# Kernel optimization log

Measured on AMD Instinct MI355X. Metric: run time of the kernel, lower is better.

## Reference

```python
import jax, jax.numpy as jnp
import numpy as np

B, S, D, H = 2, 2048, 1024, 16
HD = D // H            # head_dim = 64
CHUNK = 1024           # hard-coded in the torch module
ROPE_THETA = 10000.0


def setup_inputs() -> dict:
    key = jax.random.key(0)
    ks = jax.random.split(key, 5)
    hidden_states = jax.random.normal(ks[0], (B, S, D), dtype=jnp.float32)
    # Precomputed RoPE frequencies: freqs_cis[s, j] = exp(i * s * theta_j),
    # stored as real [S, HD//2, 2] = (cos, sin).
    inv_freq = 1.0 / (ROPE_THETA ** (np.arange(0, HD, 2, dtype=np.float32) / HD))
    ang = np.outer(np.arange(S, dtype=np.float32), inv_freq)  # [S, HD//2]
    freqs_cis = jnp.stack([jnp.cos(ang), jnp.sin(ang)], axis=-1).astype(jnp.float32)
    scale = 0.02
    Wq = jax.random.normal(ks[1], (D, D), dtype=jnp.float32) * scale
    Wk = jax.random.normal(ks[2], (D, D), dtype=jnp.float32) * scale
    Wv = jax.random.normal(ks[3], (D, D), dtype=jnp.float32) * scale
    Wo = jax.random.normal(ks[4], (D, D), dtype=jnp.float32) * scale
    return {"hidden_states": hidden_states, "freqs_cis": freqs_cis,
            "Wq": Wq, "Wk": Wk, "Wv": Wv, "Wo": Wo}


def _apply_rope(x, freqs_cis):
    # x: [B, S, H, HD]; freqs_cis: [S, HD//2, 2] (cos, sin)
    b, s, h, hd = x.shape
    xr = x.reshape(b, s, h, hd // 2, 2)
    a, bb = xr[..., 0], xr[..., 1]
    c = freqs_cis[:s, :, 0][None, :, None, :]  # broadcast over batch, heads
    d = freqs_cis[:s, :, 1][None, :, None, :]
    # complex multiply (a + ib)(c + id)
    out = jnp.stack([a * c - bb * d, a * d + bb * c], axis=-1)
    return out.reshape(b, s, h, hd)


def reference(hidden_states, freqs_cis, Wq, Wk, Wv, Wo):
    b, s, dm = hidden_states.shape
    q = (hidden_states @ Wq).reshape(b, s, H, HD)
    k = (hidden_states @ Wk).reshape(b, s, H, HD)
    v = (hidden_states @ Wv).reshape(b, s, H, HD)
    q = _apply_rope(q, freqs_cis)
    k = _apply_rope(k, freqs_cis)
    q = q.transpose(0, 2, 1, 3)  # [B, H, S, HD]
    k = k.transpose(0, 2, 1, 3)
    v = v.transpose(0, 2, 1, 3)
    scaling = HD ** (-0.5)
    out = jnp.zeros_like(q)
    # Faithful replication of the (buggy) chunked attention: softmax is
    # normalized PER key-chunk, then chunk outputs are summed.
    for i in range(0, s, CHUNK):
        j = min(i + CHUNK, s)
        w = jnp.einsum('bhqd,bhkd->bhqk', q, k[:, :, i:j]) * scaling
        w = jax.nn.softmax(w.astype(jnp.float32), axis=-1).astype(q.dtype)
        out = out + jnp.einsum('bhqk,bhkd->bhqd', w, v[:, :, i:j])
    out = out.transpose(0, 2, 1, 3).reshape(b, s, dm)
    return out @ Wo
```

## Files before the change

kernel.cpp:

```cpp
#include <hip/hip_runtime.h>
#include <hip/hip_bf16.h>
#include <cstdint>

typedef __bf16 bf16x8 __attribute__((ext_vector_type(8)));
typedef float f32x4 __attribute__((ext_vector_type(4)));
typedef float f32x16 __attribute__((ext_vector_type(16)));

#define MFMA16(a, b, c) __builtin_amdgcn_mfma_f32_16x16x32_bf16(a, b, c, 0, 0, 0)
#define MFMA32(a, b, c) __builtin_amdgcn_mfma_f32_32x32x16_bf16(a, b, c, 0, 0, 0)

__device__ __forceinline__ void gload_lds16(const void* g, void* l) {
  __builtin_amdgcn_global_load_lds(
      (const __attribute__((address_space(1))) unsigned int*)g,
      (__attribute__((address_space(3))) unsigned int*)l, 16, 0, 0);
}

__device__ __forceinline__ unsigned short f2bf(float x) {
  union { float f; uint32_t u; } v; v.f = x;
  uint32_t r = v.u + 0x7fff + ((v.u >> 16) & 1);
  return (unsigned short)(r >> 16);
}
__device__ __forceinline__ float bf2f(unsigned short h) {
  union { float f; uint32_t u; } v; v.u = ((uint32_t)h) << 16;
  return v.f;
}
__device__ __forceinline__ f32x16 fzero16() {
  f32x16 v;
#pragma unroll
  for (int i = 0; i < 16; ++i) v[i] = 0.f;
  return v;
}

__global__ __launch_bounds__(256) void k_split(const float* __restrict__ x,
                                               unsigned short* __restrict__ hi, int n4) {
  int i = blockIdx.x * blockDim.x + threadIdx.x;
  if (i >= n4) return;
  float4 v = ((const float4*)x)[i];
  ushort4 h;
  h.x = f2bf(v.x); h.y = f2bf(v.y); h.z = f2bf(v.z); h.w = f2bf(v.w);
  ((ushort4*)hi)[i] = h;
}

__global__ __launch_bounds__(256) void k_wsplit(
    const float* __restrict__ Wq, const float* __restrict__ Wk,
    const float* __restrict__ Wv, const float* __restrict__ Wo,
    unsigned short* __restrict__ WtqH, unsigned short* __restrict__ WtkH,
    unsigned short* __restrict__ WtvH, unsigned short* __restrict__ WtoH) {
  const int z = blockIdx.z;
  const float* W = (z == 0) ? Wq : (z == 1) ? Wk : (z == 2) ? Wv : Wo;
  unsigned short* WtH = (z == 0) ? WtqH : (z == 1) ? WtkH : (z == 2) ? WtvH : WtoH;
  __shared__ float tile[32][33];
  const int bx = blockIdx.x, by = blockIdx.y;
  const int tx = threadIdx.x & 31, ty = threadIdx.x >> 5;
#pragma unroll
  for (int i = 0; i < 4; ++i)
    tile[ty + i * 8][tx] = W[(size_t)(by * 32 + ty + i * 8) * 1024 + bx * 32 + tx];
  __syncthreads();
#pragma unroll
  for (int i = 0; i < 4; ++i) {
    float v = tile[tx][ty + i * 8];
    WtH[(size_t)(bx * 32 + ty + i * 8) * 1024 + by * 32 + tx] = f2bf(v);
  }
}

__global__ __launch_bounds__(256, 2) void k_qkv(
    const unsigned short* __restrict__ hsH,
    const unsigned short* __restrict__ WqH, const unsigned short* __restrict__ WkH,
    const unsigned short* __restrict__ WvH, const float* __restrict__ freqs,
    unsigned short* __restrict__ qB, unsigned short* __restrict__ kB,
    unsigned short* __restrict__ vB) {
  __shared__ unsigned short Ah[128 * 32], Bh[128 * 32];
  const int tid = threadIdx.x;
  const int bm = blockIdx.y, bn = blockIdx.x;
  const int w = bn >> 3;
  const int n0 = (bn & 7) * 128;
  const unsigned short* WH = (w == 0) ? WqH : (w == 1) ? WkH : WvH;
  const int lane = tid & 63, wave = tid >> 6;
  const int wm = (wave & 1) * 64, wn = (wave >> 1) * 64;
  const int l15 = lane & 15, lq = lane >> 4;

  f32x4 acc[4][4];
#pragma unroll
  for (int i = 0; i < 4; i++)
#pragma unroll
    for (int j = 0; j < 4; j++) acc[i][j] = (f32x4){0.f, 0.f, 0.f, 0.f};

  const char* baseA = (const char*)hsH + (size_t)(bm * 128) * 2048;
  const char* baseB = (const char*)WH + (size_t)n0 * 2048;
  const int off0 = tid << 4, row0 = off0 >> 6, seg0 = off0 & 63;
  const int off1 = (tid + 256) << 4, row1 = off1 >> 6, seg1 = off1 & 63;

  for (int k0 = 0; k0 < 1024; k0 += 32) {
    __syncthreads();
    gload_lds16(baseA + (size_t)row0 * 2048 + k0 * 2 + seg0, (char*)Ah + wave * 1024);
    gload_lds16(baseB + (size_t)row0 * 2048 + k0 * 2 + seg0, (char*)Bh + wave * 1024);
    gload_lds16(baseA + (size_t)row1 * 2048 + k0 * 2 + seg1,
                (char*)Ah + 4096 + wave * 1024);
    gload_lds16(baseB + (size_t)row1 * 2048 + k0 * 2 + seg1,
                (char*)Bh + 4096 + wave * 1024);
    __syncthreads();
    bf16x8 ah[4], bh[4];
#pragma unroll
    for (int i = 0; i < 4; ++i) {
      ah[i] = *(const bf16x8*)&Ah[(wm + i * 16 + l15) * 32 + lq * 8];
      bh[i] = *(const bf16x8*)&Bh[(wn + i * 16 + l15) * 32 + lq * 8];
    }
#pragma unroll
    for (int i = 0; i < 4; ++i)
#pragma unroll
      for (int j = 0; j < 4; ++j) acc[i][j] = MFMA16(ah[i], bh[j], acc[i][j]);
  }

  unsigned short* dst = (w == 0) ? qB : (w == 1) ? kB : vB;
#pragma unroll
  for (int i = 0; i < 4; ++i) {
#pragma unroll
    for (int j = 0; j < 4; ++j) {
      int colw = n0 + wn + j * 16 + l15;
      int h = colw >> 6, d = colw & 63;
#pragma unroll
      for (int r = 0; r < 4; ++r) {
        int rowg = bm * 128 + wm + i * 16 + lq * 4 + r;
        int s = rowg & 2047, b = rowg >> 11;
        float val = acc[i][j][r];
        if (w < 2) {
          float partner = __shfl_xor(val, 1);
          int jj = d >> 1;
          float cs = freqs[(s * 32 + jj) * 2 + 0];
          float sn = freqs[(s * 32 + jj) * 2 + 1];
          float res = (d & 1) ? (partner * sn + val * cs) : (val * cs - partner * sn);
          dst[(((size_t)(b * 16 + h)) * 2048 + s) * 64 + d] = f2bf(res);
        } else {
          dst[(((size_t)(b * 16 + h)) * 64 + d) * 2048 + s] = f2bf(val);
        }
      }
    }
  }
}

#define LDP 72

__global__ __launch_bounds__(256, 2) void k_attn(
    const unsigned short* __restrict__ qB, const unsigned short* __restrict__ kB,
    const unsigned short* __restrict__ vB,
    unsigned short* __restrict__ c0, unsigned short* __restrict__ c1) {
  __shared__ unsigned short Pt[4 * 64 * LDP];
  const int tid = threadIdx.x, lane = tid & 63, wave = tid >> 6;
  const int l31 = lane & 31, lh = lane >> 5;
  const int bid = blockIdx.x;
  const int x = (bid >> 3) & 7;
  const int gg = (bid & 7) + 8 * (bid >> 6);
  const int bh = gg & 31;
  const int chunk = gg >> 5;
  const int q0 = x * 256 + wave * 64;
  const size_t base = (size_t)bh * 2048 * 64;
  const float sc = 0.125f * 1.44269504089f;

  bf16x8 qf[2][4];
#pragma unroll
  for (int qt = 0; qt < 2; ++qt)
#pragma unroll
    for (int ks = 0; ks < 4; ++ks)
      qf[qt][ks] = *(const bf16x8*)(qB + base + (size_t)(q0 + qt * 32 + l31) * 64 +
                                    ks * 16 + lh * 8);

  const unsigned short* kp = kB + base + (size_t)chunk * 1024 * 64 + l31 * 64 + lh * 8;
  const unsigned short* vp = vB + base + l31 * 2048 + chunk * 1024 + lh * 8;
  unsigned short* Pw = Pt + wave * (64 * LDP);

  bf16x8 kfa[4], kfb[4];
#pragma unroll
  for (int ks = 0; ks < 4; ++ks) {
    kfa[ks] = *(const bf16x8*)(kp + ks * 16);
    kfb[ks] = *(const bf16x8*)(kp + 2048 + ks * 16);
  }
  kp += 4096;

  f32x16 o[2][2];
#pragma unroll
  for (int a = 0; a < 2; ++a)
#pragma unroll
    for (int bq = 0; bq < 2; ++bq) o[a][bq] = fzero16();
  float rsum[2] = {0.f, 0.f};

  for (int kb = 0; kb < 16; ++kb) {
    bf16x8 vf[2][4];
#pragma unroll
    for (int dt = 0; dt < 2; ++dt)
#pragma unroll
      for (int ks = 0; ks < 4; ++ks)
        vf[dt][ks] = *(const bf16x8*)(vp + dt * 65536 + ks * 16);

#pragma unroll
    for (int mt = 0; mt < 2; ++mt) {
      f32x16 s0 = fzero16(), s1 = fzero16();
      if (mt == 0) {
#pragma unroll
        for (int ks = 0; ks < 4; ++ks) {
          s0 = MFMA32(kfa[ks], qf[0][ks], s0);
          s1 = MFMA32(kfa[ks], qf[1][ks], s1);
        }
#pragma unroll
        for (int ks = 0; ks < 4; ++ks) kfa[ks] = *(const bf16x8*)(kp + ks * 16);
      } else {
#pragma unroll
        for (int ks = 0; ks < 4; ++ks) {
          s0 = MFMA32(kfb[ks], qf[0][ks], s0);
          s1 = MFMA32(kfb[ks], qf[1][ks], s1);
        }
#pragma unroll
        for (int ks = 0; ks < 4; ++ks)
          kfb[ks] = *(const bf16x8*)(kp + 2048 + ks * 16);
      }
#pragma unroll
      for (int qt = 0; qt < 2; ++qt) {
        const f32x16& sv = qt ? s1 : s0;
        float ps[16];
        float rs = 0.f;
#pragma unroll
        for (int r = 0; r < 16; ++r) {
          ps[r] = __builtin_exp2f(sv[r] * sc);
          rs += ps[r];
        }
        rsum[qt] += rs;
        unsigned int* prow =
            (unsigned int*)(Pw + (qt * 32 + l31) * LDP + mt * 32 + 4 * lh);
#pragma unroll
        for (int p = 0; p < 8; ++p) {
          union { unsigned int u; __bf16 h2[2]; } pk;
          pk.h2[0] = (__bf16)ps[2 * p];
          pk.h2[1] = (__bf16)ps[2 * p + 1];
          prow[4 * (p >> 1) + (p & 1)] = pk.u;
        }
      }
    }
    kp += 4096;

#pragma unroll
    for (int qt = 0; qt < 2; ++qt)
#pragma unroll
      for (int ks = 0; ks < 4; ++ks) {
        bf16x8 pf = *(const bf16x8*)(Pw + (qt * 32 + l31) * LDP + ks * 16 + lh * 8);
        o[0][qt] = MFMA32(vf[0][ks], pf, o[0][qt]);
        o[1][qt] = MFMA32(vf[1][ks], pf, o[1][qt]);
      }
    vp += 64;
  }

  unsigned short* cB = chunk ? c1 : c0;
  const int b = bh >> 4, h = bh & 15;
#pragma unroll
  for (int qt = 0; qt < 2; ++qt) {
    float lsum = rsum[qt] + __shfl_xor(rsum[qt], 32);
    float inv = 1.f / lsum;
    int s = q0 + qt * 32 + l31;
#pragma unroll
    for (int dt = 0; dt < 2; ++dt)
#pragma unroll
      for (int g = 0; g < 4; ++g) {
        int d = dt * 32 + 4 * lh + 8 * g;
        size_t idx = ((size_t)(b * 2048 + s)) * 1024 + h * 64 + d;
        ushort4 hv;
#pragma unroll
        for (int t = 0; t < 4; ++t)
          ((unsigned short*)&hv)[t] = f2bf(o[dt][qt][g * 4 + t] * inv);
        *(ushort4*)(cB + idx) = hv;
      }
  }
}

__global__ __launch_bounds__(256) void k_comb(const unsigned short* __restrict__ c0,
                                              const unsigned short* __restrict__ c1,
                                              unsigned short* __restrict__ outB,
                                              int n8) {
  int i = blockIdx.x * blockDim.x + threadIdx.x;
  if (i >= n8) return;
  uint4 a = ((const uint4*)c0)[i];
  uint4 b = ((const uint4*)c1)[i];
  uint4 r;
  const unsigned short* pa = (const unsigned short*)&a;
  const unsigned short* pb = (const unsigned short*)&b;
  unsigned short* pr = (unsigned short*)&r;
#pragma unroll
  for (int j = 0; j < 8; ++j) pr[j] = f2bf(bf2f(pa[j]) + bf2f(pb[j]));
  ((uint4*)outB)[i] = r;
}

__global__ __launch_bounds__(256, 2) void k_out(const unsigned short* __restrict__ A,
                                                const unsigned short* __restrict__ B,
                                                float* __restrict__ out) {
  __shared__ unsigned short Ah[128 * 32], Bh[128 * 32];
  const int tid = threadIdx.x;
  const int bm = blockIdx.y, n0 = blockIdx.x * 128;
  const int lane = tid & 63, wave = tid >> 6;
  const int wm = (wave & 1) * 64, wn = (wave >> 1) * 64;
  const int l15 = lane & 15, lq = lane >> 4;

  f32x4 acc[4][4];
#pragma unroll
  for (int i = 0; i < 4; i++)
#pragma unroll
    for (int j = 0; j < 4; j++) acc[i][j] = (f32x4){0.f, 0.f, 0.f, 0.f};

  const char* baseA = (const char*)A + (size_t)(bm * 128) * 2048;
  const char* baseB = (const char*)B + (size_t)n0 * 2048;
  const int off0 = tid << 4, row0 = off0 >> 6, seg0 = off0 & 63;
  const int off1 = (tid + 256) << 4, row1 = off1 >> 6, seg1 = off1 & 63;

  for (int k0 = 0; k0 < 1024; k0 += 32) {
    __syncthreads();
    gload_lds16(baseA + (size_t)row0 * 2048 + k0 * 2 + seg0, (char*)Ah + wave * 1024);
    gload_lds16(baseB + (size_t)row0 * 2048 + k0 * 2 + seg0, (char*)Bh + wave * 1024);
    gload_lds16(baseA + (size_t)row1 * 2048 + k0 * 2 + seg1,
                (char*)Ah + 4096 + wave * 1024);
    gload_lds16(baseB + (size_t)row1 * 2048 + k0 * 2 + seg1,
                (char*)Bh + 4096 + wave * 1024);
    __syncthreads();
    bf16x8 ah[4], bh[4];
#pragma unroll
    for (int i = 0; i < 4; ++i) {
      ah[i] = *(const bf16x8*)&Ah[(wm + i * 16 + l15) * 32 + lq * 8];
      bh[i] = *(const bf16x8*)&Bh[(wn + i * 16 + l15) * 32 + lq * 8];
    }
#pragma unroll
    for (int i = 0; i < 4; ++i)
#pragma unroll
      for (int j = 0; j < 4; ++j) acc[i][j] = MFMA16(ah[i], bh[j], acc[i][j]);
  }
#pragma unroll
  for (int i = 0; i < 4; ++i)
#pragma unroll
    for (int j = 0; j < 4; ++j) {
      int colw = n0 + wn + j * 16 + l15;
#pragma unroll
      for (int r = 0; r < 4; ++r) {
        int rowg = bm * 128 + wm + i * 16 + lq * 4 + r;
        out[(size_t)rowg * 1024 + colw] = acc[i][j][r];
      }
    }
}

extern "C" void kernel_launch(void* const* d_in, const int* in_sizes, int n_in,
                              void* d_out, int out_size, void* d_ws, size_t ws_size,
                              hipStream_t stream) {
  const float* hs = (const float*)d_in[0];
  const float* freqs = (const float*)d_in[1];
  const float* Wq = (const float*)d_in[2];
  const float* Wk = (const float*)d_in[3];
  const float* Wv = (const float*)d_in[4];
  const float* Wo = (const float*)d_in[5];
  float* out = (float*)d_out;

  const size_t MD = (size_t)4096 * 1024;
  const size_t WW = (size_t)1024 * 1024;
  unsigned short* hsH = (unsigned short*)d_ws;
  unsigned short* WtqH = hsH + MD;
  unsigned short* WtkH = WtqH + WW;
  unsigned short* WtvH = WtkH + WW;
  unsigned short* WtoH = WtvH + WW;
  unsigned short* qB = WtoH + WW;
  unsigned short* kB = qB + MD;
  unsigned short* vB = kB + MD;
  unsigned short* c0 = vB + MD;
  unsigned short* c1 = c0 + MD;
  unsigned short* attnB = hsH;

  k_split<<<4096, 256, 0, stream>>>(hs, hsH, (int)(MD / 4));
  k_wsplit<<<dim3(32, 32, 4), 256, 0, stream>>>(Wq, Wk, Wv, Wo,
                                                WtqH, WtkH, WtvH, WtoH);
  k_qkv<<<dim3(24, 32), 256, 0, stream>>>(hsH, WtqH, WtkH, WtvH, freqs, qB, kB, vB);
  k_attn<<<512, 256, 0, stream>>>(qB, kB, vB, c0, c1);
  k_comb<<<2048, 256, 0, stream>>>(c0, c1, attnB, (int)(MD / 8));
  k_out<<<dim3(8, 32), 256, 0, stream>>>(attnB, WtoH, out);
}
```

Before: 261.0 us.

## Halve per-wave query tile in attention kernel and double grid size

Each attention wave now handles 32 query rows instead of 64, which halves the accumulator and score registers and the LDS P tile. The grid doubles to 1024 blocks and the launch bounds ask for 4 blocks per CU, raising occupancy and parallelism. In exchange every K and V fragment loaded from global memory is reused across only half as many queries, so K/V load traffic per output doubles.

```diff
diff --git a/kernel.cpp b/kernel.cpp
--- a/kernel.cpp
+++ b/kernel.cpp
@@ -140,33 +140,30 @@
 
 #define LDP 72
 
-__global__ __launch_bounds__(256, 2) void k_attn(
+__global__ __launch_bounds__(256, 4) void k_attn(
     const unsigned short* __restrict__ qB, const unsigned short* __restrict__ kB,
     const unsigned short* __restrict__ vB,
     unsigned short* __restrict__ c0, unsigned short* __restrict__ c1) {
-  __shared__ unsigned short Pt[4 * 64 * LDP];
+  __shared__ unsigned short Pt[4 * 32 * LDP];
   const int tid = threadIdx.x, lane = tid & 63, wave = tid >> 6;
   const int l31 = lane & 31, lh = lane >> 5;
   const int bid = blockIdx.x;
-  const int x = (bid >> 3) & 7;
-  const int gg = (bid & 7) + 8 * (bid >> 6);
+  const int x = (bid >> 3) & 15;
+  const int gg = (bid & 7) + 8 * (bid >> 7);
   const int bh = gg & 31;
   const int chunk = gg >> 5;
-  const int q0 = x * 256 + wave * 64;
+  const int q0 = x * 128 + wave * 32;
   const size_t base = (size_t)bh * 2048 * 64;
   const float sc = 0.125f * 1.44269504089f;
 
-  bf16x8 qf[2][4];
-#pragma unroll
-  for (int qt = 0; qt < 2; ++qt)
-#pragma unroll
-    for (int ks = 0; ks < 4; ++ks)
-      qf[qt][ks] = *(const bf16x8*)(qB + base + (size_t)(q0 + qt * 32 + l31) * 64 +
-                                    ks * 16 + lh * 8);
+  bf16x8 qf[4];
+#pragma unroll
+  for (int ks = 0; ks < 4; ++ks)
+    qf[ks] = *(const bf16x8*)(qB + base + (size_t)(q0 + l31) * 64 + ks * 16 + lh * 8);
 
   const unsigned short* kp = kB + base + (size_t)chunk * 1024 * 64 + l31 * 64 + lh * 8;
   const unsigned short* vp = vB + base + l31 * 2048 + chunk * 1024 + lh * 8;
-  unsigned short* Pw = Pt + wave * (64 * LDP);
+  unsigned short* Pw = Pt + wave * (32 * LDP);
 
   bf16x8 kfa[4], kfb[4];
 #pragma unroll
@@ -176,12 +173,10 @@
   }
   kp += 4096;
 
-  f32x16 o[2][2];
-#pragma unroll
-  for (int a = 0; a < 2; ++a)
-#pragma unroll
-    for (int bq = 0; bq < 2; ++bq) o[a][bq] = fzero16();
-  float rsum[2] = {0.f, 0.f};
+  f32x16 o[2];
+#pragma unroll
+  for (int a = 0; a < 2; ++a) o[a] = fzero16();
+  float rsum = 0.f;
 
   for (int kb = 0; kb < 16; ++kb) {
     bf16x8 vf[2][4];
@@ -193,80 +188,64 @@
 
 #pragma unroll
     for (int mt = 0; mt < 2; ++mt) {
-      f32x16 s0 = fzero16(), s1 = fzero16();
+      f32x16 s0 = fzero16();
       if (mt == 0) {
 #pragma unroll
-        for (int ks = 0; ks < 4; ++ks) {
-          s0 = MFMA32(kfa[ks], qf[0][ks], s0);
-          s1 = MFMA32(kfa[ks], qf[1][ks], s1);
-        }
+        for (int ks = 0; ks < 4; ++ks) s0 = MFMA32(kfa[ks], qf[ks], s0);
 #pragma unroll
         for (int ks = 0; ks < 4; ++ks) kfa[ks] = *(const bf16x8*)(kp + ks * 16);
       } else {
 #pragma unroll
-        for (int ks = 0; ks < 4; ++ks) {
-          s0 = MFMA32(kfb[ks], qf[0][ks], s0);
-          s1 = MFMA32(kfb[ks], qf[1][ks], s1);
-        }
+        for (int ks = 0; ks < 4; ++ks) s0 = MFMA32(kfb[ks], qf[ks], s0);
 #pragma unroll
         for (int ks = 0; ks < 4; ++ks)
           kfb[ks] = *(const bf16x8*)(kp + 2048 + ks * 16);
       }
-#pragma unroll
-      for (int qt = 0; qt < 2; ++qt) {
-        const f32x16& sv = qt ? s1 : s0;
-        float ps[16];
-        float rs = 0.f;
-#pragma unroll
-        for (int r = 0; r < 16; ++r) {
-          ps[r] = __builtin_exp2f(sv[r] * sc);
-          rs += ps[r];
-        }
-        rsum[qt] += rs;
-        unsigned int* prow =
-            (unsigned int*)(Pw + (qt * 32 + l31) * LDP + mt * 32 + 4 * lh);
-#pragma unroll
-        for (int p = 0; p < 8; ++p) {
-          union { unsigned int u; __bf16 h2[2]; } pk;
-          pk.h2[0] = (__bf16)ps[2 * p];
-          pk.h2[1] = (__bf16)ps[2 * p + 1];
-          prow[4 * (p >> 1) + (p & 1)] = pk.u;
-        }
+      float ps[16];
+      float rs = 0.f;
+#pragma unroll
+      for (int r = 0; r < 16; ++r) {
+        ps[r] = __builtin_exp2f(s0[r] * sc);
+        rs += ps[r];
+      }
+      rsum += rs;
+      unsigned int* prow = (unsigned int*)(Pw + l31 * LDP + mt * 32 + 4 * lh);
+#pragma unroll
+      for (int p = 0; p < 8; ++p) {
+        union { unsigned int u; __bf16 h2[2]; } pk;
+        pk.h2[0] = (__bf16)ps[2 * p];
+        pk.h2[1] = (__bf16)ps[2 * p + 1];
+        prow[4 * (p >> 1) + (p & 1)] = pk.u;
       }
     }
     kp += 4096;
 
 #pragma unroll
-    for (int qt = 0; qt < 2; ++qt)
-#pragma unroll
-      for (int ks = 0; ks < 4; ++ks) {
-        bf16x8 pf = *(const bf16x8*)(Pw + (qt * 32 + l31) * LDP + ks * 16 + lh * 8);
-        o[0][qt] = MFMA32(vf[0][ks], pf, o[0][qt]);
-        o[1][qt] = MFMA32(vf[1][ks], pf, o[1][qt]);
-      }
+    for (int ks = 0; ks < 4; ++ks) {
+      bf16x8 pf = *(const bf16x8*)(Pw + l31 * LDP + ks * 16 + lh * 8);
+      o[0] = MFMA32(vf[0][ks], pf, o[0]);
+      o[1] = MFMA32(vf[1][ks], pf, o[1]);
+    }
     vp += 64;
   }
 
   unsigned short* cB = chunk ? c1 : c0;
   const int b = bh >> 4, h = bh & 15;
-#pragma unroll
-  for (int qt = 0; qt < 2; ++qt) {
-    float lsum = rsum[qt] + __shfl_xor(rsum[qt], 32);
-    float inv = 1.f / lsum;
-    int s = q0 + qt * 32 + l31;
-#pragma unroll
-    for (int dt = 0; dt < 2; ++dt)
-#pragma unroll
-      for (int g = 0; g < 4; ++g) {
-        int d = dt * 32 + 4 * lh + 8 * g;
-        size_t idx = ((size_t)(b * 2048 + s)) * 1024 + h * 64 + d;
-        ushort4 hv;
-#pragma unroll
-        for (int t = 0; t < 4; ++t)
-          ((unsigned short*)&hv)[t] = f2bf(o[dt][qt][g * 4 + t] * inv);
-        *(ushort4*)(cB + idx) = hv;
-      }
-  }
+  float lsum = rsum + __shfl_xor(rsum, 32);
+  float inv = 1.f / lsum;
+  int s = q0 + l31;
+#pragma unroll
+  for (int dt = 0; dt < 2; ++dt)
+#pragma unroll
+    for (int g = 0; g < 4; ++g) {
+      int d = dt * 32 + 4 * lh + 8 * g;
+      size_t idx = ((size_t)(b * 2048 + s)) * 1024 + h * 64 + d;
+      ushort4 hv;
+#pragma unroll
+      for (int t = 0; t < 4; ++t)
+        ((unsigned short*)&hv)[t] = f2bf(o[dt][g * 4 + t] * inv);
+      *(ushort4*)(cB + idx) = hv;
+    }
 }
 
 __global__ __launch_bounds__(256) void k_comb(const unsigned short* __restrict__ c0,
@@ -369,7 +348,7 @@
   k_wsplit<<<dim3(32, 32, 4), 256, 0, stream>>>(Wq, Wk, Wv, Wo,
                                                 WtqH, WtkH, WtvH, WtoH);
   k_qkv<<<dim3(24, 32), 256, 0, stream>>>(hsH, WtqH, WtkH, WtvH, freqs, qB, kB, vB);
-  k_attn<<<512, 256, 0, stream>>>(qB, kB, vB, c0, c1);
+  k_attn<<<1024, 256, 0, stream>>>(qB, kB, vB, c0, c1);
   k_comb<<<2048, 256, 0, stream>>>(c0, c1, attnB, (int)(MD / 8));
   k_out<<<dim3(8, 32), 256, 0, stream>>>(attnB, WtoH, out);
 }
```

Result: slower. 324.6 us (+24.4%).

## Feed softmax probabilities directly from registers to PV MFMA via permuted V layout

Applied to the files above, without the earlier changes.

The attention kernel no longer round-trips the probability tile through LDS. The V tensor is written with a permuted sequence index (bits 2 and 3 swapped), so the QK^T MFMA accumulator layout matches the B-operand layout needed by the PV MFMA. The softmax scale (1/8·log2e) is folded into Q at projection time, which removes a multiply per score. This cuts LDS writes, LDS reads and the associated waits, at the cost of a fragile layout coupling between the projection and attention kernels.

```diff
diff --git a/kernel.cpp b/kernel.cpp
--- a/kernel.cpp
+++ b/kernel.cpp
@@ -29,6 +29,23 @@
 #pragma unroll
   for (int i = 0; i < 16; ++i) v[i] = 0.f;
   return v;
+}
+
+__device__ __forceinline__ void ptrans(const f32x16& sv, float& rsum,
+                                       bf16x8& f0, bf16x8& f1) {
+  float ps[16];
+#pragma unroll
+  for (int r = 0; r < 16; ++r) ps[r] = __builtin_exp2f(sv[r]);
+  float rs = 0.f;
+#pragma unroll
+  for (int r = 0; r < 16; ++r) rs += ps[r];
+  rsum += rs;
+  bf16x8 a, b;
+#pragma unroll
+  for (int r = 0; r < 8; ++r) a[r] = (__bf16)ps[r];
+#pragma unroll
+  for (int r = 0; r < 8; ++r) b[r] = (__bf16)ps[8 + r];
+  f0 = a; f1 = b;
 }
 
 __global__ __launch_bounds__(256) void k_split(const float* __restrict__ x,
@@ -129,22 +146,21 @@
           float cs = freqs[(s * 32 + jj) * 2 + 0];
           float sn = freqs[(s * 32 + jj) * 2 + 1];
           float res = (d & 1) ? (partner * sn + val * cs) : (val * cs - partner * sn);
+          if (w == 0) res *= 0.18033688011112042f;
           dst[(((size_t)(b * 16 + h)) * 2048 + s) * 64 + d] = f2bf(res);
         } else {
-          dst[(((size_t)(b * 16 + h)) * 64 + d) * 2048 + s] = f2bf(val);
+          int sp = (s & ~12) | ((s & 4) << 1) | ((s & 8) >> 1);
+          dst[(((size_t)(b * 16 + h)) * 64 + d) * 2048 + sp] = f2bf(val);
         }
       }
     }
   }
 }
-
-#define LDP 72
 
 __global__ __launch_bounds__(256, 2) void k_attn(
     const unsigned short* __restrict__ qB, const unsigned short* __restrict__ kB,
     const unsigned short* __restrict__ vB,
     unsigned short* __restrict__ c0, unsigned short* __restrict__ c1) {
-  __shared__ unsigned short Pt[4 * 64 * LDP];
   const int tid = threadIdx.x, lane = tid & 63, wave = tid >> 6;
   const int l31 = lane & 31, lh = lane >> 5;
   const int bid = blockIdx.x;
@@ -154,7 +170,6 @@
   const int chunk = gg >> 5;
   const int q0 = x * 256 + wave * 64;
   const size_t base = (size_t)bh * 2048 * 64;
-  const float sc = 0.125f * 1.44269504089f;
 
   bf16x8 qf[2][4];
 #pragma unroll
@@ -166,7 +181,6 @@
 
   const unsigned short* kp = kB + base + (size_t)chunk * 1024 * 64 + l31 * 64 + lh * 8;
   const unsigned short* vp = vB + base + l31 * 2048 + chunk * 1024 + lh * 8;
-  unsigned short* Pw = Pt + wave * (64 * LDP);
 
   bf16x8 kfa[4], kfb[4];
 #pragma unroll
@@ -191,59 +205,49 @@
       for (int ks = 0; ks < 4; ++ks)
         vf[dt][ks] = *(const bf16x8*)(vp + dt * 65536 + ks * 16);
 
-#pragma unroll
-    for (int mt = 0; mt < 2; ++mt) {
+    bf16x8 f0, f1;
+    {
       f32x16 s0 = fzero16(), s1 = fzero16();
-      if (mt == 0) {
-#pragma unroll
-        for (int ks = 0; ks < 4; ++ks) {
-          s0 = MFMA32(kfa[ks], qf[0][ks], s0);
-          s1 = MFMA32(kfa[ks], qf[1][ks], s1);
-        }
-#pragma unroll
-        for (int ks = 0; ks < 4; ++ks) kfa[ks] = *(const bf16x8*)(kp + ks * 16);
-      } else {
-#pragma unroll
-        for (int ks = 0; ks < 4; ++ks) {
-          s0 = MFMA32(kfb[ks], qf[0][ks], s0);
-          s1 = MFMA32(kfb[ks], qf[1][ks], s1);
-        }
-#pragma unroll
-        for (int ks = 0; ks < 4; ++ks)
-          kfb[ks] = *(const bf16x8*)(kp + 2048 + ks * 16);
-      }
-#pragma unroll
-      for (int qt = 0; qt < 2; ++qt) {
-        const f32x16& sv = qt ? s1 : s0;
-        float ps[16];
-        float rs = 0.f;
-#pragma unroll
-        for (int r = 0; r < 16; ++r) {
-          ps[r] = __builtin_exp2f(sv[r] * sc);
-          rs += ps[r];
-        }
-        rsum[qt] += rs;
-        unsigned int* prow =
-            (unsigned int*)(Pw + (qt * 32 + l31) * LDP + mt * 32 + 4 * lh);
-#pragma unroll
-        for (int p = 0; p < 8; ++p) {
-          union { unsigned int u; __bf16 h2[2]; } pk;
-          pk.h2[0] = (__bf16)ps[2 * p];
-          pk.h2[1] = (__bf16)ps[2 * p + 1];
-          prow[4 * (p >> 1) + (p & 1)] = pk.u;
-        }
-      }
+#pragma unroll
+      for (int ks = 0; ks < 4; ++ks) {
+        s0 = MFMA32(kfa[ks], qf[0][ks], s0);
+        s1 = MFMA32(kfa[ks], qf[1][ks], s1);
+      }
+#pragma unroll
+      for (int ks = 0; ks < 4; ++ks) kfa[ks] = *(const bf16x8*)(kp + ks * 16);
+      ptrans(s0, rsum[0], f0, f1);
+      o[0][0] = MFMA32(vf[0][0], f0, o[0][0]);
+      o[1][0] = MFMA32(vf[1][0], f0, o[1][0]);
+      o[0][0] = MFMA32(vf[0][1], f1, o[0][0]);
+      o[1][0] = MFMA32(vf[1][1], f1, o[1][0]);
+      ptrans(s1, rsum[1], f0, f1);
+      o[0][1] = MFMA32(vf[0][0], f0, o[0][1]);
+      o[1][1] = MFMA32(vf[1][0], f0, o[1][1]);
+      o[0][1] = MFMA32(vf[0][1], f1, o[0][1]);
+      o[1][1] = MFMA32(vf[1][1], f1, o[1][1]);
+    }
+    {
+      f32x16 s0 = fzero16(), s1 = fzero16();
+#pragma unroll
+      for (int ks = 0; ks < 4; ++ks) {
+        s0 = MFMA32(kfb[ks], qf[0][ks], s0);
+        s1 = MFMA32(kfb[ks], qf[1][ks], s1);
+      }
+#pragma unroll
+      for (int ks = 0; ks < 4; ++ks)
+        kfb[ks] = *(const bf16x8*)(kp + 2048 + ks * 16);
+      ptrans(s0, rsum[0], f0, f1);
+      o[0][0] = MFMA32(vf[0][2], f0, o[0][0]);
+      o[1][0] = MFMA32(vf[1][2], f0, o[1][0]);
+      o[0][0] = MFMA32(vf[0][3], f1, o[0][0]);
+      o[1][0] = MFMA32(vf[1][3], f1, o[1][0]);
+      ptrans(s1, rsum[1], f0, f1);
+      o[0][1] = MFMA32(vf[0][2], f0, o[0][1]);
+      o[1][1] = MFMA32(vf[1][2], f0, o[1][1]);
+      o[0][1] = MFMA32(vf[0][3], f1, o[0][1]);
+      o[1][1] = MFMA32(vf[1][3], f1, o[1][1]);
     }
     kp += 4096;
-
-#pragma unroll
-    for (int qt = 0; qt < 2; ++qt)
-#pragma unroll
-      for (int ks = 0; ks < 4; ++ks) {
-        bf16x8 pf = *(const bf16x8*)(Pw + (qt * 32 + l31) * LDP + ks * 16 + lh * 8);
-        o[0][qt] = MFMA32(vf[0][ks], pf, o[0][qt]);
-        o[1][qt] = MFMA32(vf[1][ks], pf, o[1][qt]);
-      }
     vp += 64;
   }
 
```

New measurement: 243.6 us. -6.6%, faster.
